# Kernel optimization log

Measured on AMD Instinct MI355X. Metric: run time of the kernel, lower is better.

## Reference

```python
import jax, jax.numpy as jnp
import numpy as np


def patch_merge(x):
    # [B,C,H,W] -> [B,4C,H/2,W/2], channel order [x00, x10, x01, x11]
    x0 = x[:, :, 0::2, 0::2]
    x1 = x[:, :, 1::2, 0::2]
    x2 = x[:, :, 0::2, 1::2]
    x3 = x[:, :, 1::2, 1::2]
    return jnp.concatenate([x0, x1, x2, x3], axis=1)


def patch2image(x):
    # inverse of patch_merge: [B,4C,H,W] -> [B,C,2H,2W]
    B, C4, H, W = x.shape
    C = C4 // 4
    a, b, c, d = x[:, :C], x[:, C:2 * C], x[:, 2 * C:3 * C], x[:, 3 * C:]
    even = jnp.stack([a, c], axis=-1).reshape(B, C, H, 2 * W)  # rows 0::2
    odd = jnp.stack([b, d], axis=-1).reshape(B, C, H, 2 * W)   # rows 1::2
    return jnp.stack([even, odd], axis=-2).reshape(B, C, 2 * H, 2 * W)


def dwconv3x3(x, w, b):
    # depthwise 3x3 conv, SAME padding; w: [C,1,3,3], b: [C]
    C = x.shape[1]
    y = jax.lax.conv_general_dilated(
        x, w, window_strides=(1, 1), padding='SAME',
        dimension_numbers=('NCHW', 'OIHW', 'NCHW'), feature_group_count=C)
    return y + b[None, :, None, None]


def setup_inputs() -> dict:
    key = jax.random.key(0)
    ks = jax.random.split(key, 6)
    B, C, H, W = 8, 32, 256, 256
    x = jax.random.normal(ks[0], (B, C, H, W), dtype=jnp.float32)
    wq = jax.random.normal(ks[1], (C, 1, 3, 3), dtype=jnp.float32) * 0.1
    bq = jax.random.normal(ks[2], (C,), dtype=jnp.float32) * 0.1
    wk = jax.random.normal(ks[3], (C, 1, 3, 3), dtype=jnp.float32) * 0.1
    bk = jax.random.normal(ks[4], (C,), dtype=jnp.float32) * 0.1
    w1 = jax.random.normal(ks[5], (C, C), dtype=jnp.float32) * 0.1  # 1x1 conv, no bias
    return {'x': x, 'wq': wq, 'bq': bq, 'wk': wk, 'bk': bk, 'w1': w1}


def reference(x, wq, bq, wk, bk, w1):
    Q = dwconv3x3(x, wq, bq)
    K = dwconv3x3(x, wk, bk)
    V = x
    for _ in range(4):
        Q = patch_merge(Q)
        K = patch_merge(K)
        V = patch_merge(V)
    b, c, h, w = V.shape
    Qf = Q.reshape(b, c, h * w)
    Kf = K.reshape(b, c, h * w)
    Vf = V.reshape(b, c, h * w)
    # S[b,i,j] = sum_c Q[b,c,i] K[b,c,j]; softmax over j (dim=2)
    S = jax.nn.softmax(jnp.einsum('bci,bcj->bij', Qf, Kf), axis=2)
    # E = V @ S^T
    E = jnp.einsum('bcj,bij->bci', Vf, S).reshape(b, c, h, w)
    for _ in range(4):
        E = patch2image(E)
    E = E + x
    return jnp.einsum('oi,bihw->bohw', w1, E)
```

## Files before the change

### kernel.cpp

```cpp
#include <hip/hip_runtime.h>

#define B_ 8
#define C_ 32
#define NI 256
#define C4 8192

typedef _Float16 f16;
typedef __attribute__((ext_vector_type(8))) _Float16 f16x8;
typedef __attribute__((ext_vector_type(4))) _Float16 f16x4;
typedef __attribute__((ext_vector_type(2))) _Float16 f16x2;
typedef __attribute__((ext_vector_type(4))) float f32x4;

__device__ __forceinline__ int dh_of(int t) { return (t & 1) | ((t >> 1) & 2) | ((t >> 2) & 4) | ((t >> 3) & 8); }
__device__ __forceinline__ int dw_of(int t) { return ((t >> 1) & 1) | ((t >> 2) & 2) | ((t >> 3) & 4) | ((t >> 4) & 8); }

__device__ __forceinline__ void gld16(const void* g, void* lds) {
  __builtin_amdgcn_global_load_lds(
      (const __attribute__((address_space(1))) unsigned int*)g,
      (__attribute__((address_space(3))) unsigned int*)lds, 16, 0, 0);
}

__global__ __launch_bounds__(256) void k1a_conv(
    const float* __restrict__ x, const float* __restrict__ wq, const float* __restrict__ bq,
    const float* __restrict__ wk, const float* __restrict__ bk,
    f16* __restrict__ Qn, f16* __restrict__ Kn, f16* __restrict__ Vtt)
{
  __shared__ __align__(16) float xs[19 * 260];
  const int bid = blockIdx.x;
  const int hi = bid & 15, c = (bid >> 4) & 31, b = bid >> 9;
  const int tid = threadIdx.x, wave = tid >> 6, lane = tid & 63;
  const size_t cimg = ((size_t)(b * 32 + c)) << 16;

  if (tid < 19) {
    f32x4 z = {};
    *(f32x4*)&xs[tid * 260 + 256] = z;
  }
  for (int rr = wave; rr < 18; rr += 4) {
    const int gh = hi * 16 - 1 + rr;
    if ((unsigned)gh < 256u) {
      gld16(x + cimg + (size_t)gh * 256 + lane * 4, (char*)&xs[(rr + 1) * 260]);
    } else {
      f32x4 z = {};
      *(f32x4*)&xs[(rr + 1) * 260 + lane * 4] = z;
    }
  }
  __syncthreads();

  {
    const int hl = tid >> 4, wseg = tid & 15;
    const int w0 = wseg * 16;
    float q[16], k[16];
    const float bqv = bq[c], bkv = bk[c];
#pragma unroll
    for (int w = 0; w < 16; ++w) { q[w] = bqv; k[w] = bkv; }
#pragma unroll
    for (int dy = 0; dy < 3; ++dy) {
      const float* row = &xs[(hl + 1 + dy) * 260];
      float rbuf[24];
#pragma unroll
      for (int v6 = 0; v6 < 6; ++v6) {
        const f32x4 a = *(const f32x4*)(row + w0 - 4 + 4 * v6);
#pragma unroll
        for (int e = 0; e < 4; ++e) rbuf[v6 * 4 + e] = a[e];
      }
      const float q0 = wq[c * 9 + dy * 3], q1 = wq[c * 9 + dy * 3 + 1], q2 = wq[c * 9 + dy * 3 + 2];
      const float k0 = wk[c * 9 + dy * 3], k1 = wk[c * 9 + dy * 3 + 1], k2 = wk[c * 9 + dy * 3 + 2];
#pragma unroll
      for (int w = 0; w < 16; ++w) {
        q[w] += rbuf[3 + w] * q0 + rbuf[4 + w] * q1 + rbuf[5 + w] * q2;
        k[w] += rbuf[3 + w] * k0 + rbuf[4 + w] * k1 + rbuf[5 + w] * k2;
      }
    }
    f16x8 qo[2], ko[2];
#pragma unroll
    for (int w = 0; w < 16; ++w) { qo[w >> 3][w & 7] = (f16)q[w]; ko[w >> 3][w & 7] = (f16)k[w]; }
    f16* qp = Qn + cimg + (size_t)(hi * 16 + hl) * 256 + w0;
    f16* kp = Kn + cimg + (size_t)(hi * 16 + hl) * 256 + w0;
    *(f16x8*)qp = qo[0]; *(f16x8*)(qp + 8) = qo[1];
    *(f16x8*)kp = ko[0]; *(f16x8*)(kp + 8) = ko[1];
  }

  {
    const int t = tid;
    const int dh = dh_of(t), dw = dw_of(t);
    const float* rowp = &xs[(dh + 2) * 260];
    f16x8 o0, o1;
#pragma unroll
    for (int wi = 0; wi < 16; ++wi) {
      const f16 v = (f16)rowp[wi * 16 + dw];
      if (wi < 8) o0[wi] = v; else o1[wi - 8] = v;
    }
    f16* vdst = Vtt + ((size_t)b * C4 + (size_t)t * 32 + c) * 256 + hi * 16;
    *(f16x8*)vdst = o0;
    *(f16x8*)(vdst + 8) = o1;
  }
}

__global__ __launch_bounds__(256) void k2_logits(
    const f16* __restrict__ Qn, const f16* __restrict__ Kn, float* __restrict__ Spart)
{
  __shared__ __align__(16) f16 As[64 * 64];
  __shared__ __align__(16) f16 Bs[128 * 64];
  const int tile = blockIdx.x;
  const int mt = tile >> 1, nt = tile & 1;
  const int kz = blockIdx.y, b = blockIdx.z;
  const int i0 = mt * 64, j0 = nt * 128;
  const int tid = threadIdx.x, wave = tid >> 6, lane = tid & 63;
  const int li = lane & 15, lk = lane >> 4;
  const int wm = wave >> 1, wn = wave & 1;
  const f16* Qb = Qn + ((size_t)b << 21);
  const f16* Kb = Kn + ((size_t)b << 21);
  const int srow = tid >> 3, scol8 = (tid & 7) * 8;

  f32x4 acc[2][4] = {};

#define K2_RADDR(r) ((((size_t)((r) >> 4)) << 12) + (size_t)((r) & 15) * 16)
#define K2_STAGE(kk)                                                          \
  {                                                                           \
    const int c_ = (kk) >> 8, dhb_ = ((kk) >> 4) & 15;                        \
    const size_t kpart = ((size_t)c_ << 16) +                                 \
        (size_t)(dhb_ + (scol8 >> 4)) * 256 + (scol8 & 8);                    \
    _Pragma("unroll")                                                         \
    for (int j = 0; j < 2; ++j) {                                             \
      const int rg = j * 32 + srow;                                           \
      gld16(Qb + kpart + K2_RADDR(i0 + rg),                                   \
            (char*)As + j * 4096 + wave * 1024);                              \
    }                                                                         \
    _Pragma("unroll")                                                         \
    for (int j = 0; j < 4; ++j) {                                             \
      const int rg = j * 32 + srow;                                           \
      gld16(Kb + kpart + K2_RADDR(j0 + rg),                                   \
            (char*)Bs + j * 4096 + wave * 1024);                              \
    }                                                                         \
  }

  const int kbase = kz * 1024;
  K2_STAGE(kbase);
#pragma unroll
  for (int kt = 0; kt < 16; ++kt) {
    __syncthreads();
#pragma unroll
    for (int kh = 0; kh < 2; ++kh) {
      f16x8 af[2], bf[4];
#pragma unroll
      for (int mi = 0; mi < 2; ++mi)
        af[mi] = *(const f16x8*)&As[(wm * 32 + mi * 16 + li) * 64 + kh * 32 + lk * 8];
#pragma unroll
      for (int ni = 0; ni < 4; ++ni)
        bf[ni] = *(const f16x8*)&Bs[(wn * 64 + ni * 16 + li) * 64 + kh * 32 + lk * 8];
#pragma unroll
      for (int mi = 0; mi < 2; ++mi)
#pragma unroll
        for (int ni = 0; ni < 4; ++ni)
          acc[mi][ni] = __builtin_amdgcn_mfma_f32_16x16x32_f16(af[mi], bf[ni], acc[mi][ni], 0, 0, 0);
    }
    __syncthreads();
    if (kt < 15) K2_STAGE(kbase + (kt + 1) * 64);
  }
#undef K2_STAGE
#undef K2_RADDR

  float* Sp = Spart + ((size_t)kz * B_ + b) * NI * NI;
#pragma unroll
  for (int mi = 0; mi < 2; ++mi)
#pragma unroll
    for (int ni = 0; ni < 4; ++ni)
#pragma unroll
      for (int r = 0; r < 4; ++r) {
        const int ii = i0 + wm * 32 + mi * 16 + lk * 4 + r;
        const int jc = j0 + wn * 64 + ni * 16 + li;
        Sp[(size_t)ii * NI + jc] = acc[mi][ni][r];
      }
}

__global__ __launch_bounds__(256) void k3_softmax(
    const float* __restrict__ Spart, f16* __restrict__ Sh)
{
  const int row = blockIdx.x * 4 + (threadIdx.x >> 6);
  const int lane = threadIdx.x & 63;
  const size_t base = (size_t)row * NI + lane * 4;
  f32x4 v = {0.f, 0.f, 0.f, 0.f};
#pragma unroll
  for (int kt = 0; kt < 8; ++kt) {
    const f32x4 p = *(const f32x4*)(Spart + (size_t)kt * B_ * NI * NI + base);
    v[0] += p[0]; v[1] += p[1]; v[2] += p[2]; v[3] += p[3];
  }
  float m = fmaxf(fmaxf(v[0], v[1]), fmaxf(v[2], v[3]));
#pragma unroll
  for (int d = 1; d < 64; d <<= 1) m = fmaxf(m, __shfl_xor(m, d, 64));
  const float e0 = expf(v[0] - m), e1 = expf(v[1] - m), e2 = expf(v[2] - m), e3 = expf(v[3] - m);
  float s = e0 + e1 + e2 + e3;
#pragma unroll
  for (int d = 1; d < 64; d <<= 1) s += __shfl_xor(s, d, 64);
  const float inv = 1.f / s;
  f16x4 o;
  o[0] = (f16)(e0 * inv); o[1] = (f16)(e1 * inv); o[2] = (f16)(e2 * inv); o[3] = (f16)(e3 * inv);
  *(f16x4*)(Sh + (size_t)row * NI + lane * 4) = o;
}

__global__ __launch_bounds__(256) void k4_ev(
    const f16* __restrict__ Vtt, const f16* __restrict__ Sh, f16* __restrict__ Y)
{
  __shared__ __align__(16) f16 As[128 * 64];
  __shared__ __align__(16) f16 Bs[128 * 64];
  const int mt = blockIdx.x, nt = blockIdx.y, b = blockIdx.z;
  const int m0 = mt * 128, n0 = nt * 128;
  const int tid = threadIdx.x, wave = tid >> 6, lane = tid & 63;
  const int li = lane & 15, lk = lane >> 4;
  const int wm = wave >> 1, wn = wave & 1;
  const f16* Va  = Vtt + (size_t)b * C4 * NI;
  const f16* Shb = Sh + (size_t)b * NI * NI;

  const int srow = tid >> 3, scol = (tid & 7) * 8;

  f32x4 acc[4][4] = {};

#define K4_STAGE(k0)                                                          \
  {                                                                           \
    _Pragma("unroll")                                                         \
    for (int j = 0; j < 4; ++j) {                                             \
      const int rg = j * 32 + srow;                                           \
      gld16(Va + (size_t)(m0 + rg) * NI + (k0) + scol,                        \
            (char*)As + j * 4096 + wave * 1024);                              \
      gld16(Shb + (size_t)(n0 + rg) * NI + (k0) + scol,                       \
            (char*)Bs + j * 4096 + wave * 1024);                              \
    }                                                                         \
  }

  K4_STAGE(0);
#pragma unroll
  for (int kt = 0; kt < 4; ++kt) {
    __syncthreads();
#pragma unroll
    for (int kh = 0; kh < 2; ++kh) {
      f16x8 af[4], bf[4];
#pragma unroll
      for (int mi = 0; mi < 4; ++mi)
        af[mi] = *(const f16x8*)&As[(wm * 64 + mi * 16 + li) * 64 + kh * 32 + lk * 8];
#pragma unroll
      for (int ni = 0; ni < 4; ++ni)
        bf[ni] = *(const f16x8*)&Bs[(wn * 64 + ni * 16 + li) * 64 + kh * 32 + lk * 8];
#pragma unroll
      for (int mi = 0; mi < 4; ++mi)
#pragma unroll
        for (int ni = 0; ni < 4; ++ni)
          acc[mi][ni] = __builtin_amdgcn_mfma_f32_16x16x32_f16(af[mi], bf[ni], acc[mi][ni], 0, 0, 0);
    }
    __syncthreads();
    if (kt < 3) K4_STAGE((kt + 1) * 64);
  }
#undef K4_STAGE

#pragma unroll
  for (int mi = 0; mi < 4; ++mi)
#pragma unroll
    for (int ni = 0; ni < 4; ++ni) {
      const int i = n0 + wn * 64 + ni * 16 + li;
      const int m = m0 + wm * 64 + mi * 16 + lk * 4;
      const f16* vres = Va + (size_t)m * NI + i;
      f16x4 p;
#pragma unroll
      for (int r = 0; r < 4; ++r)
        p[r] = (f16)(acc[mi][ni][r] + (float)vres[(size_t)r * NI]);
      *(f16x4*)(Y + ((size_t)(b * NI + i)) * C4 + m) = p;
    }
}

__global__ __launch_bounds__(256) void k5_w1_unpermute(
    const f16* __restrict__ Y, const float* __restrict__ w1, float* __restrict__ out)
{
  __shared__ f16 w1s[32 * 32];
  const int bid = blockIdx.x;
  const int b = bid >> 8, i = bid & 255;
  const int hi = i >> 4, wi = i & 15;
  const int tid = threadIdx.x;
#pragma unroll
  for (int e = 0; e < 4; ++e) w1s[tid + 256 * e] = (f16)w1[tid + 256 * e];
  __syncthreads();

  const int wave = tid >> 6, lane = tid & 63, li = lane & 15, lk = lane >> 4;
  const f16* Yrow = Y + ((size_t)(b * NI + i)) * C4;
  const f16x8 b0 = *(const f16x8*)(&w1s[li * 32 + lk * 8]);
  const f16x8 b1 = *(const f16x8*)(&w1s[(16 + li) * 32 + lk * 8]);

#pragma unroll
  for (int q = 0; q < 4; ++q) {
    const int tt = wave * 4 + q;
    const f16x8 a = *(const f16x8*)(Yrow + (size_t)(tt * 16 + li) * 32 + lk * 8);
    f32x4 d0 = {}, d1 = {};
    d0 = __builtin_amdgcn_mfma_f32_16x16x32_f16(a, b0, d0, 0, 0, 0);
    d1 = __builtin_amdgcn_mfma_f32_16x16x32_f16(a, b1, d1, 0, 0, 0);
#pragma unroll
    for (int r = 0; r < 4; ++r) {
      const int t = tt * 16 + lk * 4 + r;
      const int dh = dh_of(t), dw = dw_of(t);
      const int h = hi * 16 + dh, w = wi * 16 + dw;
      out[(((size_t)(b * 32 + li)) * 256 + h) * 256 + w] = d0[r];
      out[(((size_t)(b * 32 + 16 + li)) * 256 + h) * 256 + w] = d1[r];
    }
  }
}

extern "C" void kernel_launch(void* const* d_in, const int* in_sizes, int n_in,
                              void* d_out, int out_size, void* d_ws, size_t ws_size,
                              hipStream_t stream)
{
  const float* x  = (const float*)d_in[0];
  const float* wq = (const float*)d_in[1];
  const float* bq = (const float*)d_in[2];
  const float* wk = (const float*)d_in[3];
  const float* bk = (const float*)d_in[4];
  const float* w1 = (const float*)d_in[5];
  float* out = (float*)d_out;
  char* ws = (char*)d_ws;

  f16*   Qn    = (f16*)(ws);
  f16*   Kn    = (f16*)(ws + 33554432);
  f16*   Vtt   = (f16*)(ws + 67108864);
  float* Spart = (float*)(ws + 100663296);
  f16*   Sh    = (f16*)(ws + 117440512);
  f16*   Y     = Qn;

  k1a_conv<<<4096, 256, 0, stream>>>(x, wq, bq, wk, bk, Qn, Kn, Vtt);
  k2_logits<<<dim3(8, 8, 8), 256, 0, stream>>>(Qn, Kn, Spart);
  k3_softmax<<<512, 256, 0, stream>>>(Spart, Sh);
  k4_ev<<<dim3(64, 2, 8), 256, 0, stream>>>(Vtt, Sh, Y);
  k5_w1_unpermute<<<2048, 256, 0, stream>>>(Y, w1, out);
}
```

Measured before the change: 133.9 us.

## Double-buffer conv kernel: each block processes four row strips with prefetch

The depthwise-conv/V-permute kernel now has each block loop over four consecutive 16-row strips instead of one. It double-buffers the LDS staging, issuing async global-to-LDS loads for the next strip while computing the current one. This amortizes block launch and the per-block load latency and overlaps memory with compute. The cost is a 4x smaller grid (1024 blocks) and double the LDS per block, which may reduce occupancy. There is also a possible LDS reuse hazard, because the buffer being loaded for strip s+1 is the one read during strip s-1 and only one barrier sits between them.

```diff
diff --git a/kernel.cpp b/kernel.cpp
--- a/kernel.cpp
+++ b/kernel.cpp
@@ -25,75 +25,91 @@
     const float* __restrict__ wk, const float* __restrict__ bk,
     f16* __restrict__ Qn, f16* __restrict__ Kn, f16* __restrict__ Vtt)
 {
-  __shared__ __align__(16) float xs[19 * 260];
+  __shared__ __align__(16) float xs[2][19 * 260];
   const int bid = blockIdx.x;
-  const int hi = bid & 15, c = (bid >> 4) & 31, b = bid >> 9;
+  const int hq = bid & 3, c = (bid >> 2) & 31, b = bid >> 7;
   const int tid = threadIdx.x, wave = tid >> 6, lane = tid & 63;
   const size_t cimg = ((size_t)(b * 32 + c)) << 16;
 
-  if (tid < 19) {
+  if (tid < 38) {
+    const int bsel = tid >= 19, r = tid - bsel * 19;
     f32x4 z = {};
-    *(f32x4*)&xs[tid * 260 + 256] = z;
-  }
-  for (int rr = wave; rr < 18; rr += 4) {
-    const int gh = hi * 16 - 1 + rr;
-    if ((unsigned)gh < 256u) {
-      gld16(x + cimg + (size_t)gh * 256 + lane * 4, (char*)&xs[(rr + 1) * 260]);
-    } else {
-      f32x4 z = {};
-      *(f32x4*)&xs[(rr + 1) * 260 + lane * 4] = z;
-    }
-  }
-  __syncthreads();
-
-  {
-    const int hl = tid >> 4, wseg = tid & 15;
-    const int w0 = wseg * 16;
-    float q[16], k[16];
-    const float bqv = bq[c], bkv = bk[c];
-#pragma unroll
-    for (int w = 0; w < 16; ++w) { q[w] = bqv; k[w] = bkv; }
-#pragma unroll
-    for (int dy = 0; dy < 3; ++dy) {
-      const float* row = &xs[(hl + 1 + dy) * 260];
-      float rbuf[24];
-#pragma unroll
-      for (int v6 = 0; v6 < 6; ++v6) {
-        const f32x4 a = *(const f32x4*)(row + w0 - 4 + 4 * v6);
-#pragma unroll
-        for (int e = 0; e < 4; ++e) rbuf[v6 * 4 + e] = a[e];
+    *(f32x4*)&xs[bsel][r * 260 + 256] = z;
+  }
+
+#define K1_STAGE(s)                                                           \
+  {                                                                           \
+    float* buf_ = xs[(s) & 1];                                                \
+    for (int rr = wave; rr < 18; rr += 4) {                                   \
+      const int gh = hq * 64 + (s) * 16 - 1 + rr;                             \
+      if ((unsigned)gh < 256u) {                                              \
+        gld16(x + cimg + (size_t)gh * 256 + lane * 4,                         \
+              (char*)&buf_[(rr + 1) * 260]);                                  \
+      } else {                                                                \
+        f32x4 z_ = {};                                                        \
+        *(f32x4*)&buf_[(rr + 1) * 260 + lane * 4] = z_;                       \
+      }                                                                       \
+    }                                                                         \
+  }
+
+  K1_STAGE(0);
+#pragma unroll
+  for (int s = 0; s < 4; ++s) {
+    __syncthreads();
+    if (s < 3) K1_STAGE(s + 1);
+    const float* bufp = xs[s & 1];
+    const int hi = hq * 4 + s;
+
+    {
+      const int hl = tid >> 4, wseg = tid & 15;
+      const int w0 = wseg * 16;
+      float q[16], k[16];
+      const float bqv = bq[c], bkv = bk[c];
+#pragma unroll
+      for (int w = 0; w < 16; ++w) { q[w] = bqv; k[w] = bkv; }
+#pragma unroll
+      for (int dy = 0; dy < 3; ++dy) {
+        const float* row = &bufp[(hl + 1 + dy) * 260];
+        float rbuf[24];
+#pragma unroll
+        for (int v6 = 0; v6 < 6; ++v6) {
+          const f32x4 a = *(const f32x4*)(row + w0 - 4 + 4 * v6);
+#pragma unroll
+          for (int e = 0; e < 4; ++e) rbuf[v6 * 4 + e] = a[e];
+        }
+        const float q0 = wq[c * 9 + dy * 3], q1 = wq[c * 9 + dy * 3 + 1], q2 = wq[c * 9 + dy * 3 + 2];
+        const float k0 = wk[c * 9 + dy * 3], k1 = wk[c * 9 + dy * 3 + 1], k2 = wk[c * 9 + dy * 3 + 2];
+#pragma unroll
+        for (int w = 0; w < 16; ++w) {
+          q[w] += rbuf[3 + w] * q0 + rbuf[4 + w] * q1 + rbuf[5 + w] * q2;
+          k[w] += rbuf[3 + w] * k0 + rbuf[4 + w] * k1 + rbuf[5 + w] * k2;
+        }
       }
-      const float q0 = wq[c * 9 + dy * 3], q1 = wq[c * 9 + dy * 3 + 1], q2 = wq[c * 9 + dy * 3 + 2];
-      const float k0 = wk[c * 9 + dy * 3], k1 = wk[c * 9 + dy * 3 + 1], k2 = wk[c * 9 + dy * 3 + 2];
-#pragma unroll
-      for (int w = 0; w < 16; ++w) {
-        q[w] += rbuf[3 + w] * q0 + rbuf[4 + w] * q1 + rbuf[5 + w] * q2;
-        k[w] += rbuf[3 + w] * k0 + rbuf[4 + w] * k1 + rbuf[5 + w] * k2;
+      f16x8 qo[2], ko[2];
+#pragma unroll
+      for (int w = 0; w < 16; ++w) { qo[w >> 3][w & 7] = (f16)q[w]; ko[w >> 3][w & 7] = (f16)k[w]; }
+      f16* qp = Qn + cimg + (size_t)(hi * 16 + hl) * 256 + w0;
+      f16* kp = Kn + cimg + (size_t)(hi * 16 + hl) * 256 + w0;
+      *(f16x8*)qp = qo[0]; *(f16x8*)(qp + 8) = qo[1];
+      *(f16x8*)kp = ko[0]; *(f16x8*)(kp + 8) = ko[1];
+    }
+
+    {
+      const int t = tid;
+      const int dh = dh_of(t), dw = dw_of(t);
+      const float* rowp = &bufp[(dh + 2) * 260];
+      f16x8 o0, o1;
+#pragma unroll
+      for (int wi = 0; wi < 16; ++wi) {
+        const f16 v = (f16)rowp[wi * 16 + dw];
+        if (wi < 8) o0[wi] = v; else o1[wi - 8] = v;
       }
-    }
-    f16x8 qo[2], ko[2];
-#pragma unroll
-    for (int w = 0; w < 16; ++w) { qo[w >> 3][w & 7] = (f16)q[w]; ko[w >> 3][w & 7] = (f16)k[w]; }
-    f16* qp = Qn + cimg + (size_t)(hi * 16 + hl) * 256 + w0;
-    f16* kp = Kn + cimg + (size_t)(hi * 16 + hl) * 256 + w0;
-    *(f16x8*)qp = qo[0]; *(f16x8*)(qp + 8) = qo[1];
-    *(f16x8*)kp = ko[0]; *(f16x8*)(kp + 8) = ko[1];
-  }
-
-  {
-    const int t = tid;
-    const int dh = dh_of(t), dw = dw_of(t);
-    const float* rowp = &xs[(dh + 2) * 260];
-    f16x8 o0, o1;
-#pragma unroll
-    for (int wi = 0; wi < 16; ++wi) {
-      const f16 v = (f16)rowp[wi * 16 + dw];
-      if (wi < 8) o0[wi] = v; else o1[wi - 8] = v;
-    }
-    f16* vdst = Vtt + ((size_t)b * C4 + (size_t)t * 32 + c) * 256 + hi * 16;
-    *(f16x8*)vdst = o0;
-    *(f16x8*)(vdst + 8) = o1;
-  }
+      f16* vdst = Vtt + ((size_t)b * C4 + (size_t)t * 32 + c) * 256 + hi * 16;
+      *(f16x8*)vdst = o0;
+      *(f16x8*)(vdst + 8) = o1;
+    }
+  }
+#undef K1_STAGE
 }
 
 __global__ __launch_bounds__(256) void k2_logits(
@@ -321,7 +337,7 @@
   f16*   Sh    = (f16*)(ws + 117440512);
   f16*   Y     = Qn;
 
-  k1a_conv<<<4096, 256, 0, stream>>>(x, wq, bq, wk, bk, Qn, Kn, Vtt);
+  k1a_conv<<<1024, 256, 0, stream>>>(x, wq, bq, wk, bk, Qn, Kn, Vtt);
   k2_logits<<<dim3(8, 8, 8), 256, 0, stream>>>(Qn, Kn, Spart);
   k3_softmax<<<512, 256, 0, stream>>>(Spart, Sh);
   k4_ev<<<dim3(64, 2, 8), 256, 0, stream>>>(Vtt, Sh, Y);
```

After: 132.7 us. About the same (-0.9%).

## Widen EV GEMM tile to full N and stage w1 output in LDS

Applied to the files above, without the earlier changes.

Each k4_ev block now computes a 128x256 output tile covering the whole softmax dimension, doubling the accumulators and the B staging buffer. This halves the number of V tile reloads and the grid size. k5 now writes its 1x1-conv results into a padded LDS tile and then writes 16-float contiguous row segments to the output with vector stores, replacing scattered 4-byte global writes. The cost is more LDS and registers per block (lower occupancy) and fewer k4 blocks to fill the GPU; the padded LDS rows also make the 16-byte LDS reads unaligned for odd channel rows.

```diff
diff --git a/kernel.cpp b/kernel.cpp
--- a/kernel.cpp
+++ b/kernel.cpp
@@ -202,9 +202,9 @@
     const f16* __restrict__ Vtt, const f16* __restrict__ Sh, f16* __restrict__ Y)
 {
   __shared__ __align__(16) f16 As[128 * 64];
-  __shared__ __align__(16) f16 Bs[128 * 64];
-  const int mt = blockIdx.x, nt = blockIdx.y, b = blockIdx.z;
-  const int m0 = mt * 128, n0 = nt * 128;
+  __shared__ __align__(16) f16 Bs[256 * 64];
+  const int mt = blockIdx.x, b = blockIdx.y;
+  const int m0 = mt * 128;
   const int tid = threadIdx.x, wave = tid >> 6, lane = tid & 63;
   const int li = lane & 15, lk = lane >> 4;
   const int wm = wave >> 1, wn = wave & 1;
@@ -213,18 +213,18 @@
 
   const int srow = tid >> 3, scol = (tid & 7) * 8;
 
-  f32x4 acc[4][4] = {};
+  f32x4 acc[4][8] = {};
 
 #define K4_STAGE(k0)                                                          \
   {                                                                           \
     _Pragma("unroll")                                                         \
-    for (int j = 0; j < 4; ++j) {                                             \
-      const int rg = j * 32 + srow;                                           \
-      gld16(Va + (size_t)(m0 + rg) * NI + (k0) + scol,                        \
+    for (int j = 0; j < 4; ++j)                                               \
+      gld16(Va + (size_t)(m0 + j * 32 + srow) * NI + (k0) + scol,             \
             (char*)As + j * 4096 + wave * 1024);                              \
-      gld16(Shb + (size_t)(n0 + rg) * NI + (k0) + scol,                       \
+    _Pragma("unroll")                                                         \
+    for (int j = 0; j < 8; ++j)                                               \
+      gld16(Shb + (size_t)(j * 32 + srow) * NI + (k0) + scol,                 \
             (char*)Bs + j * 4096 + wave * 1024);                              \
-    }                                                                         \
   }
 
   K4_STAGE(0);
@@ -233,18 +233,22 @@
     __syncthreads();
 #pragma unroll
     for (int kh = 0; kh < 2; ++kh) {
-      f16x8 af[4], bf[4];
+      f16x8 af[4];
 #pragma unroll
       for (int mi = 0; mi < 4; ++mi)
         af[mi] = *(const f16x8*)&As[(wm * 64 + mi * 16 + li) * 64 + kh * 32 + lk * 8];
 #pragma unroll
-      for (int ni = 0; ni < 4; ++ni)
-        bf[ni] = *(const f16x8*)&Bs[(wn * 64 + ni * 16 + li) * 64 + kh * 32 + lk * 8];
-#pragma unroll
-      for (int mi = 0; mi < 4; ++mi)
-#pragma unroll
-        for (int ni = 0; ni < 4; ++ni)
-          acc[mi][ni] = __builtin_amdgcn_mfma_f32_16x16x32_f16(af[mi], bf[ni], acc[mi][ni], 0, 0, 0);
+      for (int nq = 0; nq < 2; ++nq) {
+        f16x8 bf[4];
+#pragma unroll
+        for (int nn = 0; nn < 4; ++nn)
+          bf[nn] = *(const f16x8*)&Bs[(wn * 128 + (nq * 4 + nn) * 16 + li) * 64 + kh * 32 + lk * 8];
+#pragma unroll
+        for (int mi = 0; mi < 4; ++mi)
+#pragma unroll
+          for (int nn = 0; nn < 4; ++nn)
+            acc[mi][nq * 4 + nn] = __builtin_amdgcn_mfma_f32_16x16x32_f16(af[mi], bf[nn], acc[mi][nq * 4 + nn], 0, 0, 0);
+      }
     }
     __syncthreads();
     if (kt < 3) K4_STAGE((kt + 1) * 64);
@@ -254,8 +258,8 @@
 #pragma unroll
   for (int mi = 0; mi < 4; ++mi)
 #pragma unroll
-    for (int ni = 0; ni < 4; ++ni) {
-      const int i = n0 + wn * 64 + ni * 16 + li;
+    for (int ni = 0; ni < 8; ++ni) {
+      const int i = wn * 128 + ni * 16 + li;
       const int m = m0 + wm * 64 + mi * 16 + lk * 4;
       const f16* vres = Va + (size_t)m * NI + i;
       f16x4 p;
@@ -269,6 +273,7 @@
 __global__ __launch_bounds__(256) void k5_w1_unpermute(
     const f16* __restrict__ Y, const float* __restrict__ w1, float* __restrict__ out)
 {
+  __shared__ float os[32 * 257];
   __shared__ f16 w1s[32 * 32];
   const int bid = blockIdx.x;
   const int b = bid >> 8, i = bid & 255;
@@ -294,10 +299,22 @@
     for (int r = 0; r < 4; ++r) {
       const int t = tt * 16 + lk * 4 + r;
       const int dh = dh_of(t), dw = dw_of(t);
-      const int h = hi * 16 + dh, w = wi * 16 + dw;
-      out[(((size_t)(b * 32 + li)) * 256 + h) * 256 + w] = d0[r];
-      out[(((size_t)(b * 32 + 16 + li)) * 256 + h) * 256 + w] = d1[r];
-    }
+      os[li * 257 + dh * 16 + dw] = d0[r];
+      os[(16 + li) * 257 + dh * 16 + dw] = d1[r];
+    }
+  }
+  __syncthreads();
+
+  const size_t ob = (((size_t)b * 32) << 16) + (size_t)(hi * 16) * 256 + wi * 16;
+#pragma unroll
+  for (int e = 0; e < 2; ++e) {
+    const int rid = tid + 256 * e;
+    const int o = rid >> 4, dh = rid & 15;
+    const float* src = &os[o * 257 + dh * 16];
+    float* dst = out + ob + (((size_t)o) << 16) + (size_t)dh * 256;
+#pragma unroll
+    for (int v4 = 0; v4 < 4; ++v4)
+      *(f32x4*)(dst + v4 * 4) = *(const f32x4*)(src + v4 * 4);
   }
 }
 
@@ -324,6 +341,6 @@
   k1a_conv<<<4096, 256, 0, stream>>>(x, wq, bq, wk, bk, Qn, Kn, Vtt);
   k2_logits<<<dim3(8, 8, 8), 256, 0, stream>>>(Qn, Kn, Spart);
   k3_softmax<<<512, 256, 0, stream>>>(Spart, Sh);
-  k4_ev<<<dim3(64, 2, 8), 256, 0, stream>>>(Vtt, Sh, Y);
+  k4_ev<<<dim3(64, 8), 256, 0, stream>>>(Vtt, Sh, Y);
   k5_w1_unpermute<<<2048, 256, 0, stream>>>(Y, w1, out);
 }
```

Result: no change. 133.7 us (-0.1%).
